# Kernel optimization log

Measured on AMD Instinct MI355X. Metric: run time of the kernel, lower is better.

## Reference

```python
import jax, jax.numpy as jnp
import numpy as np

SR = 16000; NFFT = 1024; HOP = 256; NMELS = 80; GRUH = 256; ZDIM = 16
NBINS = 65; HID = 512; B = 8; TLEN = 160000; PAD = NFFT // 2; IRLEN = 8000

def _consts():
    freqs = np.linspace(0, SR / 2, NFFT // 2 + 1); fsq = freqs ** 2
    aw = (12194.217 ** 2 * fsq ** 2) / ((fsq + 20.6 ** 2) * (fsq + 107.7 ** 2) * (fsq + 737.9 ** 2) * (fsq + 12194.217 ** 2) ** 0.5 + 1e-8)
    h2m = lambda f: 2595.0 * np.log10(1.0 + f / 700.0)
    m2h = lambda m: 700.0 * (10.0 ** (m / 2595.0) - 1.0)
    f_pts = m2h(np.linspace(h2m(0.0), h2m(SR / 2.0), NMELS + 2))
    fd = f_pts[1:] - f_pts[:-1]
    sl = f_pts[None, :] - freqs[:, None]
    fb = np.maximum(0.0, np.minimum(-sl[:, :-2] / fd[:-1], sl[:, 2:] / fd[1:]))
    win = 0.5 - 0.5 * np.cos(2.0 * np.pi * np.arange(NFFT) / NFFT)  # periodic hann
    return jnp.asarray(aw, jnp.float32), jnp.asarray(fb, jnp.float32), jnp.asarray(win, jnp.float32)
AW, MELFB, WIN = _consts()

def _frame(x, size, hop):
    n = (x.shape[-1] - size) // hop + 1
    idx = jnp.arange(n)[:, None] * hop + jnp.arange(size)[None, :]
    return x[:, idx]

def _stft(x):  # [B,T] -> [B, n_frames, 513] complex
    xp = jnp.pad(x, ((0, 0), (PAD, PAD)), mode='reflect')
    return jnp.fft.rfft(_frame(xp, NFFT, HOP) * WIN, axis=-1)

def _istft(spec, length):  # [B, n_frames, 513] -> [B, length]
    fr = jnp.fft.irfft(spec, n=NFFT, axis=-1) * WIN
    n = fr.shape[1]; total = (n - 1) * HOP + NFFT
    idx = (jnp.arange(n)[:, None] * HOP + jnp.arange(NFFT)[None, :]).reshape(-1)
    out = jnp.zeros((fr.shape[0], total), fr.dtype).at[:, idx].add(fr.reshape(fr.shape[0], -1))
    wsq = jnp.zeros((total,), WIN.dtype).at[idx].add(jnp.tile(WIN ** 2, (n,)))
    out = out / jnp.where(wsq > 1e-11, wsq, 1.0)
    return out[:, PAD:PAD + length]

def _lin_interp(x, size):  # torch F.interpolate(mode='linear', align_corners=False) on last axis
    L = x.shape[-1]
    pos = jnp.clip((jnp.arange(size) + 0.5) * (L / size) - 0.5, 0.0, L - 1.0)
    lo = jnp.floor(pos).astype(jnp.int32); hi = jnp.minimum(lo + 1, L - 1); w = pos - lo
    return x[..., lo] * (1.0 - w) + x[..., hi] * w

def _gru(x, wih, whh, bih, bhh):  # torch nn.GRU, batch_first, h0=0
    xp = x @ wih.T + bih
    def step(h, xt):
        gh = h @ whh.T + bhh
        xr, xz, xn = jnp.split(xt, 3, -1); hr, hz, hn = jnp.split(gh, 3, -1)
        r = jax.nn.sigmoid(xr + hr); z = jax.nn.sigmoid(xz + hz)
        nn_ = jnp.tanh(xn + r * hn)
        h = (1.0 - z) * nn_ + z * h
        return h, h
    h0 = jnp.zeros((x.shape[0], whh.shape[1]), x.dtype)
    _, hs = jax.lax.scan(step, h0, jnp.swapaxes(xp, 0, 1))
    return jnp.swapaxes(hs, 0, 1)

def _forward(audio, gender, age, gru_wih, gru_whh, gru_bih, gru_bhh, proj_w, proj_b,
             w0, b0, g0, e0, w1, b1, g1, e1, w2, b2, g2, e2,
             oq_w, oq_b, vt_w, vt_b, nf_w, nf_b, ir):
    # --- pitch via autocorrelation ---
    xp = jnp.pad(audio, ((0, 0), (PAD, PAD)), mode='reflect')
    fr = _frame(xp, NFFT, HOP)
    ps = jnp.abs(jnp.fft.rfft(fr, n=2 * NFFT, axis=-1)) ** 2
    ac = jnp.fft.irfft(ps, n=2 * NFFT, axis=-1)[..., :NFFT]
    ac = ac / (ac[..., :1] + 1e-8)
    min_lag, max_lag = SR // 1000, SR // 50  # 16, 320
    reg = ac[..., min_lag:max_lag]
    mv = jnp.max(reg, -1); mi = jnp.argmax(reg, -1)
    f0 = SR / (mi.astype(jnp.float32) + min_lag + 1e-8)
    f0 = jnp.where(mv < 0.3, 0.0, f0)[..., None]  # [B,F,1]
    # --- loudness + mels ---
    spec = jnp.abs(_stft(audio)) ** 2  # [B,F,513]
    loud = 10.0 * jnp.log10(jnp.mean((spec + 1e-8) * AW, -1, keepdims=True))  # [B,F,1]
    mels = jnp.log(spec @ MELFB + 1e-5)  # [B,F,80]
    mels = (mels - mels.mean(1, keepdims=True)) / jnp.sqrt(mels.var(1, keepdims=True) + 1e-5)
    z = _gru(mels, gru_wih, gru_whh, gru_bih, gru_bhh) @ proj_w.T + proj_b  # [B,F,16]
    Fn = f0.shape[1]
    # --- controller ---
    gb = jnp.broadcast_to(gender[:, None, :], (gender.shape[0], Fn, 2))
    ab = jnp.broadcast_to(age[:, None, :], (age.shape[0], Fn, 1))
    h = jnp.concatenate([z, (jnp.log(f0 + 1e-5) - 4.0) / 4.0, loud / 100.0 + 1.0, gb, ab], -1)
    for W, bb, gm, bt in ((w0, b0, g0, e0), (w1, b1, g1, e1), (w2, b2, g2, e2)):
        h = h @ W.T + bb
        h = (h - h.mean(-1, keepdims=True)) / jnp.sqrt(h.var(-1, keepdims=True) + 1e-5) * gm + bt
        h = jnp.where(h >= 0, h, 0.1 * h)  # LeakyReLU(0.1)
    oq = jax.nn.sigmoid(h @ oq_w.T + oq_b)
    vt = jax.nn.sigmoid(h @ vt_w.T + vt_b)
    nf = jax.nn.sigmoid(h @ nf_w.T + nf_b)
    amp = 10.0 ** (loud / 20.0)
    # --- decoder ---
    L = audio.shape[-1]
    f0u = _lin_interp(f0[..., 0], L); ampu = _lin_interp(amp[..., 0], L); oqu = _lin_interp(oq[..., 0], L)
    phase = jnp.cumsum(f0u / SR, -1); p = phase - jnp.floor(phase)
    oqc = jnp.clip(oqu, 0.1, 0.9)
    pulse = 0.5 * (1.0 - jnp.cos(jnp.pi * p / (oqc + 1e-8)))
    g = pulse * jax.nn.sigmoid((oqc - p) * 100.0)
    glottal = jnp.pad(g[..., 1:] - g[..., :-1], ((0, 0), (1, 0)))
    noise = jax.random.normal(jax.random.key(42), glottal.shape, glottal.dtype)
    def apply_filter(ex, filt):
        es = _stft(ex)  # [B,nf,513]
        ft = _lin_interp(jnp.swapaxes(filt, 1, 2), es.shape[1])  # time interp
        ff = _lin_interp(jnp.swapaxes(ft, 1, 2), es.shape[2])    # bin interp 65->513
        return _istft(es * ff, L)
    dry = (apply_filter(glottal, vt) + apply_filter(noise, nf)) * ampu
    # --- FFT reverb ---
    nconv = int(2 ** int(np.ceil(np.log2(L + IRLEN - 1))))
    wet = jnp.fft.irfft(jnp.fft.rfft(dry, n=nconv) * jnp.fft.rfft(ir, n=nconv), n=nconv)[..., :L]
    return wet, dry

def setup_inputs() -> dict:
    ks = iter(jax.random.split(jax.random.key(0), 48))
    def nrm(shape, s=0.05):
        return jax.random.normal(next(ks), shape, jnp.float32) * s
    inp = {}
    inp['audio'] = jax.random.normal(next(ks), (B, TLEN), jnp.float32)
    inp['gender'] = jax.random.uniform(next(ks), (B, 2), jnp.float32)
    inp['age'] = jax.random.uniform(next(ks), (B, 1), jnp.float32)
    inp['gru_wih'] = nrm((3 * GRUH, NMELS)); inp['gru_whh'] = nrm((3 * GRUH, GRUH))
    inp['gru_bih'] = jnp.zeros((3 * GRUH,), jnp.float32); inp['gru_bhh'] = jnp.zeros((3 * GRUH,), jnp.float32)
    inp['proj_w'] = nrm((ZDIM, GRUH)); inp['proj_b'] = jnp.zeros((ZDIM,), jnp.float32)
    din = ZDIM + 5
    inp['w0'] = nrm((HID, din)); inp['b0'] = jnp.zeros((HID,), jnp.float32)
    inp['g0'] = jnp.ones((HID,), jnp.float32); inp['e0'] = jnp.zeros((HID,), jnp.float32)
    inp['w1'] = nrm((HID, HID)); inp['b1'] = jnp.zeros((HID,), jnp.float32)
    inp['g1'] = jnp.ones((HID,), jnp.float32); inp['e1'] = jnp.zeros((HID,), jnp.float32)
    inp['w2'] = nrm((HID, HID)); inp['b2'] = jnp.zeros((HID,), jnp.float32)
    inp['g2'] = jnp.ones((HID,), jnp.float32); inp['e2'] = jnp.zeros((HID,), jnp.float32)
    inp['oq_w'] = nrm((1, HID)); inp['oq_b'] = jnp.zeros((1,), jnp.float32)
    inp['vt_w'] = nrm((NBINS, HID)); inp['vt_b'] = jnp.zeros((NBINS,), jnp.float32)
    inp['nf_w'] = nrm((NBINS, HID)); inp['nf_b'] = jnp.zeros((NBINS,), jnp.float32)
    decay = jnp.exp(-jnp.linspace(0.0, 5.0, IRLEN))
    inp['ir'] = jax.random.normal(next(ks), (IRLEN,), jnp.float32) * 0.1 * decay
    return inp

def reference(audio, gender, age, gru_wih, gru_whh, gru_bih, gru_bhh, proj_w, proj_b,
              w0, b0, g0, e0, w1, b1, g1, e1, w2, b2, g2, e2,
              oq_w, oq_b, vt_w, vt_b, nf_w, nf_b, ir):
    return _forward(audio, gender, age, gru_wih, gru_whh, gru_bih, gru_bhh, proj_w, proj_b,
                    w0, b0, g0, e0, w1, b1, g1, e1, w2, b2, g2, e2,
                    oq_w, oq_b, vt_w, vt_b, nf_w, nf_b, ir)
```

## Files before the change

kernel.cpp:

```cpp
#include <hip/hip_runtime.h>
#include <math.h>

#define SRF 16000.0f
#define HOP 256
#define FRM 626
#define BB 8
#define TLEN 160000
#define NFRM (BB*FRM)
#define NCONV 262144
#define ACCLEN 161024
#define GCH 40

constexpr size_t oWIN   = 0;
constexpr size_t oTW    = oWIN + 1024;
constexpr size_t oDIAG  = oTW + 1024;
constexpr size_t oTWF   = oDIAG + 16;
constexpr size_t oTWC   = oTWF + 1024;
constexpr size_t oAW    = oTWC + 1024;
constexpr size_t oMELFB = oAW + 513;
constexpr size_t oWSQI  = oMELFB + 513*80;
constexpr size_t oWIHT  = oWSQI + ACCLEN;
constexpr size_t oW0T   = oWIHT + 80*768;
constexpr size_t oW1T   = oW0T + 21*512;
constexpr size_t oW2T   = oW1T + 512*512;
constexpr size_t oVTT   = oW2T + 512*512;
constexpr size_t oNFT   = oVTT + 512*65;
constexpr size_t oF0    = oNFT + 512*65;
constexpr size_t oLOUD  = oF0 + NFRM;
constexpr size_t oOQ    = oLOUD + NFRM;
constexpr size_t oVT    = oOQ + NFRM;
constexpr size_t oNF    = oVT + (size_t)NFRM*65;
constexpr size_t oGLOT  = oNF + (size_t)NFRM*65;
constexpr size_t oNOISE = oGLOT + (size_t)BB*TLEN;
constexpr size_t oACC   = oNOISE + (size_t)BB*TLEN;
constexpr size_t oCONVA = oACC + (size_t)BB*ACCLEN;
constexpr size_t oEND   = oCONVA + (size_t)5*NCONV*2;
constexpr size_t oXP    = oEND;
constexpr size_t oGSUM  = oXP + (size_t)NFRM*768;
constexpr size_t oGPRE  = oGSUM + 320;
constexpr size_t oEND2  = oGPRE + 640;
constexpr size_t oCONVB = oWSQI;
constexpr size_t oMEL = oCONVA;
constexpr size_t oHS  = oMEL + (size_t)NFRM*80;

constexpr long R_WIN=1024, R_TW=512, R_TWF=512, R_TWC=512, R_AW=513, R_MELFB=41040,
  R_WSQI=161024, R_WIHT=61440, R_W0T=10752, R_W1T=262144, R_W2T=262144,
  R_VTT=33280, R_NFT=33280, R_IR=NCONV;
constexpr long INIT_TOTAL = R_WIN+R_TW+R_TWF+R_TWC+R_AW+R_MELFB+R_WSQI+R_WIHT+R_W0T+
  R_W1T+R_W2T+R_VTT+R_NFT+R_IR;

constexpr int NOISEB = 313;
constexpr int ZACCB  = 315;
constexpr int MEGA_BLOCKS = 1 + NFRM + NOISEB + ZACCB;

typedef float f32x4 __attribute__((ext_vector_type(4)));
typedef __bf16 bf16x8 __attribute__((ext_vector_type(8)));
typedef short short8 __attribute__((ext_vector_type(8)));
#define MFMA_BF16 __builtin_amdgcn_mfma_f32_16x16x32_bf16

__device__ inline int mirror_idx(int j) {
  if (j < 0) j = -j;
  if (j >= TLEN) j = 2*TLEN - 2 - j;
  return j;
}
__device__ inline float sigm(float x) { return 1.0f/(1.0f + expf(-x)); }
__device__ inline unsigned short f2bf(float x) {
  unsigned u = __float_as_uint(x);
  return (unsigned short)((u + 0x7FFFu + ((u >> 16) & 1u)) >> 16);
}
__device__ inline float tanh_fast(float x) {
  return 1.0f - 2.0f/(__expf(2.0f*x) + 1.0f);
}

__device__ inline float interpF(const float* v, int i) {
  float pos = ((float)i + 0.5f) * (626.0f/160000.0f) - 0.5f;
  pos = fminf(fmaxf(pos, 0.0f), 625.0f);
  int lo = (int)floorf(pos);
  int hi = min(lo + 1, 625);
  float w = pos - (float)lo;
  return v[lo]*(1.0f - w) + v[hi]*w;
}
__device__ inline float interp65(const float* v, int k) {
  float pos = ((float)k + 0.5f) * (65.0f/513.0f) - 0.5f;
  pos = fminf(fmaxf(pos, 0.0f), 64.0f);
  int lo = (int)floorf(pos);
  int hi = min(lo + 1, 64);
  float w = pos - (float)lo;
  return v[lo]*(1.0f - w) + v[hi]*w;
}
__device__ inline float gwave(float ph, float oqu) {
  float p = ph - floorf(ph);
  float oqc = fminf(fmaxf(oqu, 0.1f), 0.9f);
  float pulse = 0.5f*(1.0f - cosf(3.14159265358979f * p / (oqc + 1e-8f)));
  float gs = 1.0f/(1.0f + __expf(-(oqc - p)*100.0f));
  return pulse*gs;
}

template<int LOGN, int TS>
__device__ inline void fft2(float2* c, const float2* tw, int tid, int nthr, bool inv) {
  constexpr int N = 1 << LOGN;
  for (int s = 1; s <= LOGN; ++s) {
    const int half = 1 << (s-1);
    const int tstep = (N >> s) * TS;
    for (int bf = tid; bf < (N>>1); bf += nthr) {
      int jj = bf & (half-1);
      int i0 = ((bf >> (s-1)) << s) + jj;
      int i1 = i0 + half;
      float2 wv = tw[jj*tstep];
      float wi = inv ? -wv.y : wv.y;
      float2 u = c[i0], v = c[i1];
      float tr  = v.x*wv.x - v.y*wi;
      float tci = v.x*wi  + v.y*wv.x;
      c[i0] = make_float2(u.x + tr, u.y + tci);
      c[i1] = make_float2(u.x - tr, u.y - tci);
    }
    __syncthreads();
  }
}

__device__ inline void threefry2x32(unsigned k0, unsigned k1, unsigned x0, unsigned x1,
                                    unsigned& o0, unsigned& o1) {
  unsigned ks2 = k0 ^ k1 ^ 0x1BD11BDAu;
  x0 += k0; x1 += k1;
#define TF_R(r) { x0 += x1; x1 = (x1<<(r)) | (x1>>(32-(r))); x1 ^= x0; }
  TF_R(13) TF_R(15) TF_R(26) TF_R(6)
  x0 += k1; x1 += ks2 + 1u;
  TF_R(17) TF_R(29) TF_R(16) TF_R(24)
  x0 += ks2; x1 += k0 + 2u;
  TF_R(13) TF_R(15) TF_R(26) TF_R(6)
  x0 += k0; x1 += k1 + 3u;
  TF_R(17) TF_R(29) TF_R(16) TF_R(24)
  x0 += k1; x1 += ks2 + 4u;
  TF_R(13) TF_R(15) TF_R(26) TF_R(6)
  x0 += ks2; x1 += k0 + 5u;
#undef TF_R
  o0 = x0; o1 = x1;
}

__device__ inline float erfinv_f(float x) {
  float w = -log1pf(-x*x);
  float p;
  if (w < 5.0f) {
    w = w - 2.5f;
    p = 2.81022636e-08f;
    p = fmaf(p, w, 3.43273939e-07f);
    p = fmaf(p, w, -3.5233877e-06f);
    p = fmaf(p, w, -4.39150654e-06f);
    p = fmaf(p, w, 0.00021858087f);
    p = fmaf(p, w, -0.00125372503f);
    p = fmaf(p, w, -0.00417768164f);
    p = fmaf(p, w, 0.246640727f);
    p = fmaf(p, w, 1.50140941f);
  } else {
    w = sqrtf(w) - 3.0f;
    p = -0.000200214257f;
    p = fmaf(p, w, 0.000100950558f);
    p = fmaf(p, w, 0.00134934322f);
    p = fmaf(p, w, -0.00367342844f);
    p = fmaf(p, w, 0.00573950773f);
    p = fmaf(p, w, -0.0076224613f);
    p = fmaf(p, w, 0.00943887047f);
    p = fmaf(p, w, 1.00167406f);
    p = fmaf(p, w, 2.83297682f);
  }
  return p*x;
}
__device__ inline float normal_from_bits(unsigned bits) {
  float f = __uint_as_float((bits >> 9) | 0x3F800000u) - 1.0f;
  float x = fmaxf(-0.99999994f, fmaf(f, 1.99999994f, -0.99999994f));
  return 1.41421356237f * erfinv_f(x);
}

__device__ inline double mel_fpt(int j) {
  double mmax = 2595.0 * log10(1.0 + 8000.0/700.0);
  return 700.0 * (pow(10.0, (mmax * (double)j / 81.0) / 2595.0) - 1.0);
}

__global__ void k_init(float* W, const float* wih, const float* w0,
                       const float* w1, const float* w2, const float* vtw, const float* nfw,
                       const float* ir) {
  long id = (long)blockIdx.x*256 + threadIdx.x;
  if (id < R_WIN) {
    double w = 0.5 - 0.5*cos(2.0*M_PI*(double)id/1024.0);
    W[oWIN+id] = (float)w; return;
  } id -= R_WIN;
  if (id < R_TW) {
    double a = -2.0*M_PI*(double)id/1024.0;
    W[oTW+2*id] = (float)cos(a); W[oTW+2*id+1] = (float)sin(a); return;
  } id -= R_TW;
  if (id < R_TWF) {
    double a = -2.0*M_PI*(double)id/262144.0;
    W[oTWF+2*id] = (float)cos(a); W[oTWF+2*id+1] = (float)sin(a); return;
  } id -= R_TWF;
  if (id < R_TWC) {
    double a = -2.0*M_PI*(double)id/512.0;
    W[oTWC+2*id] = (float)cos(a); W[oTWC+2*id+1] = (float)sin(a); return;
  } id -= R_TWC;
  if (id < R_AW) {
    double fr = (double)id*(8000.0/512.0); double fsq = fr*fr;
    double num = 12194.217*12194.217*fsq*fsq;
    double den = (fsq+20.6*20.6)*(fsq+107.7*107.7)*(fsq+737.9*737.9)*sqrt(fsq+12194.217*12194.217) + 1e-8;
    W[oAW+id] = (float)(num/den); return;
  } id -= R_AW;
  if (id < R_MELFB) {
    int k = (int)(id/80), m = (int)(id%80);
    double fk = (double)k*(8000.0/512.0);
    double f0p = mel_fpt(m), f1p = mel_fpt(m+1), f2p = mel_fpt(m+2);
    double lower = (fk - f0p)/(f1p - f0p);
    double upper = (f2p - fk)/(f2p - f1p);
    double v = fmax(0.0, fmin(lower, upper));
    W[oMELFB+id] = (float)v; return;
  } id -= R_MELFB;
  if (id < R_WSQI) {
    int t = (int)id;
    int n1 = t/256; if (n1 > 625) n1 = 625;
    int n0t = t - 1023 + 255; int n0 = (n0t > 0) ? n0t/256 : 0;
    double s = 0.0;
    for (int n = n0; n <= n1; ++n) {
      int o = t - n*256;
      double wv = 0.5 - 0.5*cos(2.0*M_PI*(double)o/1024.0);
      s += wv*wv;
    }
    float sf = (float)s;
    W[oWSQI+t] = (sf > 1e-11f) ? (1.0f/sf) : 1.0f; return;
  } id -= R_WSQI;
  if (id < R_WIHT) { long k = id/768, g = id%768; W[oWIHT+id] = wih[g*80+k];  return; } id -= R_WIHT;
  if (id < R_W0T)  { long d = id/512, j = id%512; W[oW0T+id] = w0[j*21+d];   return; } id -= R_W0T;
  if (id < R_W1T)  { long k = id/512, j = id%512; W[oW1T+id] = w1[j*512+k];  return; } id -= R_W1T;
  if (id < R_W2T)  { long k = id/512, j = id%512; W[oW2T+id] = w2[j*512+k];  return; } id -= R_W2T;
  if (id < R_VTT)  { long k = id/65,  m = id%65;  W[oVTT+id] = vtw[m*512+k]; return; } id -= R_VTT;
  if (id < R_NFT)  { long k = id/65,  m = id%65;  W[oNFT+id] = nfw[m*512+k]; return; } id -= R_NFT;
  if (id < R_IR) {
    size_t base = oCONVA + 2*((size_t)4*NCONV + id);
    W[base] = (id < 8000) ? ir[id] : 0.0f; W[base+1] = 0.0f; return;
  }
}

__global__ __launch_bounds__(256) void k_stft_mel(const float* audio, float* W) {
  int blk = blockIdx.x; int b = blk/FRM, f = blk%FRM; int tid = threadIdx.x;
  __shared__ float2 cb[1024];
  __shared__ float spec[513];
  __shared__ float redbuf[4];
  const float* arow = audio + (size_t)b*TLEN;
  const float2* tw = (const float2*)(W + oTW);
  for (int i = tid; i < 1024; i += 256) {
    float v = arow[mirror_idx(f*256 + i - 512)] * W[oWIN + i];
    int pos = __brev((unsigned)i) >> 22;
    cb[pos] = make_float2(v, 0.f);
  }
  __syncthreads();
  fft2<10,1>(cb, tw, tid, 256, false);
  for (int k = tid; k < 513; k += 256) { float2 z = cb[k]; spec[k] = z.x*z.x + z.y*z.y; }
  __syncthreads();
  float part = 0.f;
  for (int k = tid; k < 513; k += 256) part += (spec[k] + 1e-8f) * W[oAW + k];
  for (int off = 32; off; off >>= 1) part += __shfl_down(part, off, 64);
  if ((tid & 63) == 0) redbuf[tid >> 6] = part;
  __syncthreads();
  if (tid == 0) {
    float s = redbuf[0]+redbuf[1]+redbuf[2]+redbuf[3];
    W[oLOUD + blk] = 10.0f * log10f(s / 513.0f);
  }
  for (int m = tid; m < 80; m += 256) {
    double f0p = mel_fpt(m), f2p = mel_fpt(m + 2);
    int klo = (int)(f0p * (512.0/8000.0)); if (klo < 0) klo = 0;
    int khi = (int)(f2p * (512.0/8000.0)) + 1; if (khi > 512) khi = 512;
    float s = 0.f;
    for (int k = klo; k <= khi; ++k) s += spec[k]*W[oMELFB + (size_t)k*80 + m];
    W[oMEL + (size_t)blk*80 + m] = logf(s + 1e-5f);
  }
}

__global__ void k_melnorm(float* W) {
  int id = blockIdx.x*256 + threadIdx.x;
  if (id >= BB*80) return;
  int b = id/80, m = id%80;
  double s = 0.0, ss = 0.0;
  for (int f = 0; f < FRM; ++f) {
    double v = W[oMEL + ((size_t)b*FRM + f)*80 + m];
    s += v; ss += v*v;
  }
  double mean = s/FRM;
  double var = ss/FRM - mean*mean;
  float mu = (float)mean;
  float rstd = (float)(1.0/sqrt(var + 1e-5));
  for (int f = 0; f < FRM; ++f) {
    size_t idx = oMEL + ((size_t)b*FRM + f)*80 + m;
    W[idx] = (W[idx] - mu)*rstd;
  }
}

__global__ void k_xp(float* W, const float* bih) {
  size_t id = (size_t)blockIdx.x*256 + threadIdx.x;
  if (id >= (size_t)NFRM*768) return;
  int g = (int)(id % 768);
  size_t q = id / 768;
  const float* mrow = W + oMEL + q*80;
  float acc = bih[g];
  for (int k = 0; k < 80; ++k) acc = fmaf(mrow[k], W[oWIHT + (size_t)k*768 + g], acc);
  W[oXP + q*768 + g] = acc;
}

__global__ __launch_bounds__(512, 2) void k_mega(float* W, const float* audio,
                                                 const float* whh, const float* bhh) {
  __shared__ unsigned short sB[32768];
  __shared__ unsigned short sA[4096];
  __shared__ float sGT[9216];
  __shared__ float fr4[4][1032];
  __shared__ float wpow[8];
  __shared__ float wmax[8];
  __shared__ int   wmaxi[8];
  int tid = threadIdx.x;
  int blk = blockIdx.x;

  if (blk == 0) {
    int w = tid >> 6, l = tid & 63;
    const float* XP = W + oXP;
    float* HS = W + oHS;

    for (int idx = tid; idx < 32768; idx += 512) {
      int lcol = idx >> 8, k = idx & 255;
      int gcol = 96*(lcol >> 4) + 80 + (lcol & 15);
      sB[lcol*256 + (k ^ ((lcol & 7) << 3))] = f2bf(whh[(size_t)gcol*256 + k]);
    }
    for (int idx = tid; idx < 4096; idx += 512) sA[idx] = 0;

    int cl = l & 15, khalf = (l >> 4) * 8;
    bf16x8 bw[40];
    #pragma unroll
    for (int t2 = 0; t2 < 5; ++t2) {
      int col = 96*w + 16*t2 + cl;
      #pragma unroll
      for (int kk = 0; kk < 8; ++kk) {
        const float* src = whh + (size_t)col*256 + kk*32 + khalf;
        short8 tmp;
        #pragma unroll
        for (int j = 0; j < 8; ++j) tmp[j] = (short)f2bf(src[j]);
        bw[t2*8 + kk] = __builtin_bit_cast(bf16x8, tmp);
      }
    }

    int g = tid & 255, bbase = tid >> 8;
    float bh_r = bhh[g], bh_z = bhh[256 + g], bh_n = bhh[512 + g];
    float hprev[4] = {0.f, 0.f, 0.f, 0.f};
    int aXor = (cl & 7) << 3;
    int lcol5 = w*16 + cl;
    int rowg = l >> 4;
    int colb = 96*w + cl;
    int gtw = colb*12 + rowg*4;
    int gtr0 = g*12 + 4*bbase;
    int gtr1 = (256 + g)*12 + 4*bbase;
    int gtr2 = (512 + g)*12 + 4*bbase;

    __syncthreads();

#define LDA(kk) (*(const bf16x8*)&sA[(cl)*256 + (((kk)*32 + khalf) ^ aXor)])
#define LDB(kk) (*(const bf16x8*)&sB[(lcol5)*256 + (((kk)*32 + khalf) ^ aXor)])
#define STEPK(A_, kk) \
      c0 = MFMA_BF16(A_, bw[0*8+(kk)], c0, 0, 0, 0); \
      c1 = MFMA_BF16(A_, bw[1*8+(kk)], c1, 0, 0, 0); \
      c2 = MFMA_BF16(A_, bw[2*8+(kk)], c2, 0, 0, 0); \
      c3 = MFMA_BF16(A_, bw[3*8+(kk)], c3, 0, 0, 0); \
      c4 = MFMA_BF16(A_, bw[4*8+(kk)], c4, 0, 0, 0); \
      c5 = MFMA_BF16(A_, LDB(kk), c5, 0, 0, 0);

    for (int t = 0; t < FRM; ++t) {
      float xr[4], xz[4], xn[4];
      #pragma unroll
      for (int j = 0; j < 4; ++j) {
        const float* xpp = XP + ((size_t)(4*bbase + j)*FRM + t)*768 + g;
        xr[j] = xpp[0]; xz[j] = xpp[256]; xn[j] = xpp[512];
      }
      f32x4 c0 = {0,0,0,0}, c1 = {0,0,0,0}, c2 = {0,0,0,0};
      f32x4 c3 = {0,0,0,0}, c4 = {0,0,0,0}, c5 = {0,0,0,0};
      bf16x8 a0 = LDA(0), a1 = LDA(1), a2 = LDA(2), a3 = LDA(3);
      STEPK(a0, 0) STEPK(a1, 1) STEPK(a2, 2) STEPK(a3, 3)
      a0 = LDA(4); a1 = LDA(5); a2 = LDA(6); a3 = LDA(7);
      STEPK(a0, 4) STEPK(a1, 5) STEPK(a2, 6) STEPK(a3, 7)
      if (rowg < 3) {
        *(f32x4*)&sGT[gtw + 0*192]  = c0;
        *(f32x4*)&sGT[gtw + 1*192]  = c1;
        *(f32x4*)&sGT[gtw + 2*192]  = c2;
        *(f32x4*)&sGT[gtw + 3*192]  = c3;
        *(f32x4*)&sGT[gtw + 4*192]  = c4;
        *(f32x4*)&sGT[gtw + 5*192]  = c5;
      }
      __syncthreads();
      f32x4 rv = *(const f32x4*)&sGT[gtr0];
      f32x4 zv = *(const f32x4*)&sGT[gtr1];
      f32x4 nv = *(const f32x4*)&sGT[gtr2];
      #pragma unroll
      for (int j = 0; j < 4; ++j) {
        int bb = 4*bbase + j;
        float r = 1.0f/(1.0f + __expf(-(xr[j] + rv[j] + bh_r)));
        float z = 1.0f/(1.0f + __expf(-(xz[j] + zv[j] + bh_z)));
        float nn = tanh_fast(xn[j] + r*(nv[j] + bh_n));
        float h = (1.0f - z)*nn + z*hprev[j];
        hprev[j] = h;
        HS[((size_t)bb*FRM + t)*256 + g] = h;
        sA[bb*256 + (g ^ ((bb & 7) << 3))] = f2bf(h);
      }
      __syncthreads();
    }
#undef LDA
#undef LDB
#undef STEPK
    return;
  }
  blk -= 1;

  if (blk < NFRM) {
    int b = blk/FRM, f = blk%FRM;
    const float* arow = audio + (size_t)b*TLEN;
    for (int idx = tid; idx < 4*1032; idx += 512) {
      int s = idx/1032, i = idx - s*1032;
      int j = i + s;
      fr4[s][i] = (j < 1024) ? arow[mirror_idx(f*256 + j - 512)] : 0.f;
    }
    __syncthreads();
    int lane = tid & 63, wv = tid >> 6;
    float p = 0.f;
    for (int i = tid; i < 1024; i += 512) { float x = fr4[0][i]; p += x*x; }
    for (int off = 32; off; off >>= 1) p += __shfl_down(p, off, 64);
    if (lane == 0) wpow[wv] = p;
    float vbest = -1e30f; int ibest = tid;
    if (tid < 304) {
      int lag = 16 + tid;
      int s = lag & 3, base = lag - s;
      int qmax = (1023 - lag) >> 2;
      float acc = 0.f;
      for (int q = 0; q <= qmax; ++q) {
        float4 u = *(const float4*)&fr4[0][4*q];
        float4 v = *(const float4*)&fr4[s][base + 4*q];
        acc += u.x*v.x + u.y*v.y + u.z*v.z + u.w*v.w;
      }
      vbest = acc;
    }
    for (int off = 32; off; off >>= 1) {
      float v2 = __shfl_down(vbest, off, 64);
      int i2 = __shfl_down(ibest, off, 64);
      if (v2 > vbest || (v2 == vbest && i2 < ibest)) { vbest = v2; ibest = i2; }
    }
    if (lane == 0) { wmax[wv] = vbest; wmaxi[wv] = ibest; }
    __syncthreads();
    if (tid == 0) {
      float ac0 = 0.f;
      #pragma unroll
      for (int q = 0; q < 8; ++q) ac0 += wpow[q];
      float bv = wmax[0]; int bi = wmaxi[0];
      #pragma unroll
      for (int q = 1; q < 8; ++q) {
        if (wmax[q] > bv || (wmax[q] == bv && wmaxi[q] < bi)) { bv = wmax[q]; bi = wmaxi[q]; }
      }
      float inv = 1.0f/(ac0 + 1e-8f);
      float best = bv*inv;
      W[oF0 + (size_t)blk] = (best < 0.3f) ? 0.0f : (SRF/(float)(bi + 16));
    }
    return;
  }
  blk -= NFRM;

  if (blk < NOISEB) {
    size_t base = (size_t)blk*4096;
    #pragma unroll
    for (int j = 0; j < 8; ++j) {
      size_t p = base + (size_t)j*512 + tid;
      if (p < (size_t)BB*TLEN) {
        unsigned o0, o1;
        threefry2x32(0u, 42u, 0u, (unsigned)p, o0, o1);
        W[oNOISE + p] = normal_from_bits(o0 ^ o1);
      }
    }
    return;
  }
  blk -= NOISEB;

  {
    size_t base = (size_t)blk*4096;
    #pragma unroll
    for (int j = 0; j < 8; ++j) {
      size_t p = base + (size_t)j*512 + tid;
      if (p < (size_t)BB*ACCLEN) W[oACC + p] = 0.0f;
    }
  }
}

__device__ inline void ln_lrelu(float acc[8], float gj, float ej, float out[8][512],
                                float wred[8][8][2], float stat[8][2],
                                int tid, int lane, int wv, int j) {
  #pragma unroll
  for (int i = 0; i < 8; ++i) {
    float s = acc[i], ss = acc[i]*acc[i];
    for (int off = 32; off; off >>= 1) { s += __shfl_down(s, off, 64); ss += __shfl_down(ss, off, 64); }
    if (lane == 0) { wred[i][wv][0] = s; wred[i][wv][1] = ss; }
  }
  __syncthreads();
  if (tid < 8) {
    float s = 0.f, ss = 0.f;
    #pragma unroll
    for (int w = 0; w < 8; ++w) { s += wred[tid][w][0]; ss += wred[tid][w][1]; }
    float mean = s/512.0f;
    float var = ss/512.0f - mean*mean;
    stat[tid][0] = mean;
    stat[tid][1] = 1.0f/sqrtf(var + 1e-5f);
  }
  __syncthreads();
  #pragma unroll
  for (int i = 0; i < 8; ++i) {
    float v = (acc[i] - stat[i][0])*stat[i][1]*gj + ej;
    out[i][j] = (v >= 0.f) ? v : 0.1f*v;
  }
}

__global__ __launch_bounds__(512) void k_mlp(float* W, const float* gender, const float* age,
    const float* projw, const float* projb,
    const float* b0, const float* g0, const float* e0,
    const float* b1, const float* g1, const float* e1,
    const float* b2, const float* g2, const float* e2,
    const float* oqw, const float* oqb, const float* vtb, const float* nfb) {
  __shared__ float hbuf[8][256];
  __shared__ float in0[8][21];
  __shared__ float actA[8][512];
  __shared__ float actB[8][512];
  __shared__ float wred[8][8][2];
  __shared__ float stat[8][2];
  int tid = threadIdx.x; int q0 = blockIdx.x*8;
  for (int x = tid; x < 2048; x += 512) {
    int i = x >> 8, k = x & 255;
    hbuf[i][k] = W[oHS + ((size_t)(q0 + i))*256 + k];
  }
  __syncthreads();
  if (tid < 128) {
    int i = tid >> 4, zi = tid & 15;
    float a = projb[zi];
    for (int k = 0; k < 256; ++k) a = fmaf(hbuf[i][k], projw[zi*256 + k], a);
    in0[i][zi] = a;
  } else if (tid < 168) {
    int x = tid - 128; int i = x/5, d = 16 + x%5;
    int q = q0 + i; int b = q/FRM;
    float v;
    if (d == 16) v = (logf(W[oF0 + q] + 1e-5f) - 4.0f)*0.25f;
    else if (d == 17) v = W[oLOUD + q]/100.0f + 1.0f;
    else if (d == 18) v = gender[b*2];
    else if (d == 19) v = gender[b*2 + 1];
    else v = age[b];
    in0[i][d] = v;
  }
  __syncthreads();
  int j = tid, lane = tid & 63, wv = tid >> 6;
  float acc[8];
  #pragma unroll
  for (int i = 0; i < 8; ++i) acc[i] = b0[j];
  for (int d = 0; d < 21; ++d) {
    float w = W[oW0T + (size_t)d*512 + j];
    #pragma unroll
    for (int i = 0; i < 8; ++i) acc[i] = fmaf(in0[i][d], w, acc[i]);
  }
  ln_lrelu(acc, g0[j], e0[j], actA, wred, stat, tid, lane, wv, j);
  __syncthreads();
  #pragma unroll
  for (int i = 0; i < 8; ++i) acc[i] = b1[j];
  for (int k = 0; k < 512; ++k) {
    float w = W[oW1T + (size_t)k*512 + j];
    #pragma unroll
    for (int i = 0; i < 8; ++i) acc[i] = fmaf(actA[i][k], w, acc[i]);
  }
  ln_lrelu(acc, g1[j], e1[j], actB, wred, stat, tid, lane, wv, j);
  __syncthreads();
  #pragma unroll
  for (int i = 0; i < 8; ++i) acc[i] = b2[j];
  for (int k = 0; k < 512; ++k) {
    float w = W[oW2T + (size_t)k*512 + j];
    #pragma unroll
    for (int i = 0; i < 8; ++i) acc[i] = fmaf(actB[i][k], w, acc[i]);
  }
  ln_lrelu(acc, g2[j], e2[j], actA, wred, stat, tid, lane, wv, j);
  __syncthreads();
  for (int x = tid; x < 520; x += 512) {
    int i = x/65, m = x%65;
    float a = vtb[m], a2 = nfb[m];
    for (int k = 0; k < 512; ++k) {
      float h = actA[i][k];
      a  = fmaf(h, W[oVTT + (size_t)k*65 + m], a);
      a2 = fmaf(h, W[oNFT + (size_t)k*65 + m], a2);
    }
    W[oVT + (size_t)(q0+i)*65 + m] = sigm(a);
    W[oNF + (size_t)(q0+i)*65 + m] = sigm(a2);
  }
  if (tid < 8) {
    float a = oqb[0];
    for (int k = 0; k < 512; ++k) a = fmaf(actA[tid][k], oqw[k], a);
    W[oOQ + q0 + tid] = sigm(a);
  }
}

__global__ __launch_bounds__(256) void k_gsum(float* W) {
  int blk = blockIdx.x; int b = blk/GCH, c = blk%GCH; int tid = threadIdx.x;
  __shared__ float ws[4];
  const float* f0r = W + oF0 + (size_t)b*FRM;
  int i0 = c*4096 + tid*16;
  float s = 0.f;
  #pragma unroll
  for (int j = 0; j < 16; ++j) {
    int i = i0 + j;
    if (i < TLEN) s += interpF(f0r, i)*(1.0f/SRF);
  }
  for (int off = 32; off; off >>= 1) s += __shfl_down(s, off, 64);
  if ((tid & 63) == 0) ws[tid >> 6] = s;
  __syncthreads();
  if (tid == 0) W[oGSUM + (size_t)b*GCH + c] = ws[0]+ws[1]+ws[2]+ws[3];
}

__global__ void k_gscan(float* W) {
  if (blockIdx.x == 0 && threadIdx.x == 0) {
    double* P = (double*)(W + oGPRE);
    for (int b = 0; b < BB; ++b) {
      double a = 0.0;
      for (int c = 0; c < GCH; ++c) {
        P[b*GCH + c] = a;
        a += (double)W[oGSUM + (size_t)b*GCH + c];
      }
    }
  }
}

__global__ __launch_bounds__(256) void k_gapply(float* W) {
  int blk = blockIdx.x; int b = blk/GCH, c = blk%GCH; int tid = threadIdx.x;
  __shared__ float wss[4];
  __shared__ float lastw[4];
  const float* f0r = W + oF0 + (size_t)b*FRM;
  const float* oqr = W + oOQ + (size_t)b*FRM;
  float* grow = W + oGLOT + (size_t)b*TLEN;
  double P = ((const double*)(W + oGPRE))[b*GCH + c];
  int i0 = c*4096 + tid*16;
  int lane = tid & 63, wv = tid >> 6;
  float v[16]; float ts = 0.f;
  #pragma unroll
  for (int j = 0; j < 16; ++j) {
    int i = i0 + j;
    float x = (i < TLEN) ? interpF(f0r, i)*(1.0f/SRF) : 0.f;
    v[j] = x; ts += x;
  }
  float sc = ts;
  #pragma unroll
  for (int off = 1; off < 64; off <<= 1) {
    float o = __shfl_up(sc, off, 64);
    if (lane >= off) sc += o;
  }
  if (lane == 63) wss[wv] = sc;
  __syncthreads();
  float wpre = 0.f;
  for (int q = 0; q < wv; ++q) wpre += wss[q];
  double ph0 = P + (double)(wpre + sc - ts);
  float run = 0.f; float gq[16];
  #pragma unroll
  for (int j = 0; j < 16; ++j) {
    int i = i0 + j;
    run += v[j];
    float ph = (float)(ph0 + (double)run);
    gq[j] = gwave(ph, interpF(oqr, min(i, TLEN-1)));
  }
  float prev = __shfl_up(gq[15], 1, 64);
  if (lane == 63) lastw[wv] = gq[15];
  __syncthreads();
  if (lane == 0) {
    if (wv > 0) prev = lastw[wv - 1];
    else if (i0 > 0) prev = gwave((float)P, interpF(oqr, i0 - 1));
    else prev = 0.f;
  }
  #pragma unroll
  for (int j = 0; j < 16; ++j) {
    int i = i0 + j;
    if (i < TLEN) {
      float gl = (j == 0) ? prev : gq[j-1];
      grow[i] = (i == 0) ? 0.f : (gq[j] - gl);
    }
  }
}

__global__ __launch_bounds__(256) void k_filtsynth(float* W) {
  int blk = blockIdx.x; int b = blk/FRM, f = blk%FRM; int tid = threadIdx.x;
  __shared__ float2 cZ[1024], cS[1024];
  __shared__ float fvt[65], fnf[65];
  const float* grow = W + oGLOT + (size_t)b*TLEN;
  const float* nrow = W + oNOISE + (size_t)b*TLEN;
  const float2* tw = (const float2*)(W + oTW);
  for (int i = tid; i < 1024; i += 256) {
    int si = mirror_idx(f*256 + i - 512);
    float wv = W[oWIN + i];
    int pos = __brev((unsigned)i) >> 22;
    cZ[pos] = make_float2(grow[si]*wv, nrow[si]*wv);
  }
  if (tid < 65) {
    fvt[tid] = W[oVT + ((size_t)b*FRM + f)*65 + tid];
    fnf[tid] = W[oNF + ((size_t)b*FRM + f)*65 + tid];
  }
  __syncthreads();
  fft2<10,1>(cZ, tw, tid, 256, false);
  for (int k = tid; k <= 512; k += 256) {
    int km = (1024 - k) & 1023;
    float2 z1 = cZ[k], z2 = cZ[km];
    float Gr = 0.5f*(z1.x + z2.x), Gi = 0.5f*(z1.y - z2.y);
    float Nr = 0.5f*(z1.y + z2.y), Ni = 0.5f*(z2.x - z1.x);
    float fv = interp65(fvt, k), fn = interp65(fnf, k);
    float Sr = Gr*fv + Nr*fn, Si = Gi*fv + Ni*fn;
    cS[__brev((unsigned)k) >> 22] = make_float2(Sr, Si);
    if (km != k) cS[__brev((unsigned)km) >> 22] = make_float2(Sr, -Si);
  }
  __syncthreads();
  fft2<10,1>(cS, tw, tid, 256, true);
  float* arow = W + oACC + (size_t)b*ACCLEN + (size_t)f*256;
  for (int i = tid; i < 1024; i += 256) {
    float xv = cS[i].x*(1.0f/1024.0f)*W[oWIN + i];
    atomicAdd(arow + i, xv);
  }
}

__global__ void k_dry(float* W, float* dout) {
  size_t id = (size_t)blockIdx.x*256 + threadIdx.x;
  if (id >= (size_t)4*NCONV) return;
  int t = (int)(id / NCONV);
  int n = (int)(id % NCONV);
  float dv0 = 0.f, dv1 = 0.f;
  if (n < TLEN) {
    float pos = ((float)n + 0.5f) * (626.0f/160000.0f) - 0.5f;
    pos = fminf(fmaxf(pos, 0.0f), 625.0f);
    int lo = (int)floorf(pos);
    int hi = min(lo + 1, 625);
    float wgt = pos - (float)lo;
    float wsq = W[oWSQI + 512 + n];
    #pragma unroll
    for (int q = 0; q < 2; ++q) {
      int b = 2*t + q;
      float val = W[oACC + (size_t)b*ACCLEN + 512 + n] * wsq;
      const float* lrow = W + oLOUD + (size_t)b*FRM;
      float a0 = exp10f(lrow[lo]*0.05f);
      float a1 = exp10f(lrow[hi]*0.05f);
      float dv = val*(a0*(1.0f - wgt) + a1*wgt);
      if (q == 0) dv0 = dv; else dv1 = dv;
      dout[(size_t)BB*TLEN + (size_t)b*TLEN + n] = dv;
    }
  }
  ((float2*)(W + oCONVA))[id] = make_float2(dv0, dv1);
}

__global__ __launch_bounds__(256) void k_conv_f1(const float* in, float* out,
                                                 const float* tw, const float* twf,
                                                 const float* twc) {
  int blk = blockIdx.x; int t = blk >> 9; int bcol = blk & 511; int tid = threadIdx.x;
  __shared__ float2 cb[512];
  const float2* src = (const float2*)in + (size_t)t*NCONV;
  for (int a = tid; a < 512; a += 256) {
    int pos = __brev((unsigned)a) >> 23;
    cb[pos] = src[(size_t)a*512 + bcol];
  }
  __syncthreads();
  fft2<9,2>(cb, (const float2*)tw, tid, 256, false);
  float2* dst = (float2*)out + (size_t)t*NCONV + (size_t)bcol*512;
  for (int k1 = tid; k1 < 512; k1 += 256) {
    unsigned m = (unsigned)bcol * (unsigned)k1;
    float2 tc = ((const float2*)twc)[m >> 9];
    float2 tf = ((const float2*)twf)[m & 511];
    float wr = tc.x*tf.x - tc.y*tf.y;
    float wi = tc.x*tf.y + tc.y*tf.x;
    float2 v = cb[k1];
    dst[k1] = make_float2(v.x*wr - v.y*wi, v.x*wi + v.y*wr);
  }
}

__global__ __launch_bounds__(256) void k_conv_f2(const float* in, float* out, const float* tw) {
  int blk = blockIdx.x; int t = blk >> 9; int k1 = blk & 511; int tid = threadIdx.x;
  __shared__ float2 cb[512];
  const float2* src = (const float2*)in + (size_t)t*NCONV;
  for (int bb2 = tid; bb2 < 512; bb2 += 256) {
    int pos = __brev((unsigned)bb2) >> 23;
    cb[pos] = src[(size_t)bb2*512 + k1];
  }
  __syncthreads();
  fft2<9,2>(cb, (const float2*)tw, tid, 256, false);
  float2* dst = (float2*)out + (size_t)t*NCONV;
  for (int k2 = tid; k2 < 512; k2 += 256) {
    dst[(size_t)k1 + 512*(size_t)k2] = cb[k2];
  }
}

__global__ __launch_bounds__(256) void k_conv_f2w(const float* in, float* dout, const float* tw) {
  int blk = blockIdx.x; int t = blk >> 9; int k1 = blk & 511; int tid = threadIdx.x;
  __shared__ float2 cb[512];
  const float2* src = (const float2*)in + (size_t)t*NCONV;
  for (int bb2 = tid; bb2 < 512; bb2 += 256) {
    int pos = __brev((unsigned)bb2) >> 23;
    cb[pos] = src[(size_t)bb2*512 + k1];
  }
  __syncthreads();
  fft2<9,2>(cb, (const float2*)tw, tid, 256, false);
  float* d0 = dout + (size_t)(2*t)*TLEN;
  float* d1 = dout + (size_t)(2*t + 1)*TLEN;
  for (int k2 = tid; k2 < 512; k2 += 256) {
    int n = k1 + 512*k2;
    if (n < TLEN) {
      float2 V = cb[k2];
      d0[n] = V.x * (1.0f/262144.0f);
      d1[n] = -V.y * (1.0f/262144.0f);
    }
  }
}

__global__ void k_mul(float* W) {
  constexpr size_t HALF = NCONV/2;
  size_t id = (size_t)blockIdx.x*256 + threadIdx.x;
  if (id >= (size_t)4*(HALF + 1)) return;
  int t = (int)(id / (HALF + 1));
  size_t k = id % (HALF + 1);
  size_t km = (NCONV - k) & (NCONV - 1);
  float2* A = (float2*)(W + oCONVA);
  float2 z1 = A[(size_t)t*NCONV + k];
  float2 z2 = A[(size_t)t*NCONV + km];
  float2 c  = A[(size_t)4*NCONV + k];
  float X0r = 0.5f*(z1.x + z2.x), X0i = 0.5f*(z1.y - z2.y);
  float X1r = 0.5f*(z1.y + z2.y), X1i = 0.5f*(z2.x - z1.x);
  float P0r = X0r*c.x - X0i*c.y, P0i = X0r*c.y + X0i*c.x;
  float P1r = X1r*c.x - X1i*c.y, P1i = X1r*c.y + X1i*c.x;
  A[(size_t)t*NCONV + k] = make_float2(P0r - P1i, -(P0i + P1r));
  if (km != k) {
    A[(size_t)t*NCONV + km] = make_float2(P0r + P1i, P0i - P1r);
  }
}

extern "C" void kernel_launch(void* const* d_in, const int* in_sizes, int n_in,
                              void* d_out, int out_size, void* d_ws, size_t ws_size,
                              hipStream_t stream) {
  (void)in_sizes; (void)n_in; (void)out_size; (void)ws_size;
  const float* audio  = (const float*)d_in[0];
  const float* gender = (const float*)d_in[1];
  const float* age    = (const float*)d_in[2];
  const float* wih    = (const float*)d_in[3];
  const float* whh    = (const float*)d_in[4];
  const float* bih    = (const float*)d_in[5];
  const float* bhh    = (const float*)d_in[6];
  const float* projw  = (const float*)d_in[7];
  const float* projb  = (const float*)d_in[8];
  const float* w0     = (const float*)d_in[9];
  const float* b0     = (const float*)d_in[10];
  const float* g0     = (const float*)d_in[11];
  const float* e0     = (const float*)d_in[12];
  const float* w1     = (const float*)d_in[13];
  const float* b1     = (const float*)d_in[14];
  const float* g1     = (const float*)d_in[15];
  const float* e1     = (const float*)d_in[16];
  const float* w2     = (const float*)d_in[17];
  const float* b2     = (const float*)d_in[18];
  const float* g2     = (const float*)d_in[19];
  const float* e2     = (const float*)d_in[20];
  const float* oqw    = (const float*)d_in[21];
  const float* oqb    = (const float*)d_in[22];
  const float* vtw    = (const float*)d_in[23];
  const float* vtb    = (const float*)d_in[24];
  const float* nfw    = (const float*)d_in[25];
  const float* nfb    = (const float*)d_in[26];
  const float* ir     = (const float*)d_in[27];
  float* W = (float*)d_ws;
  float* dout = (float*)d_out;

  k_init<<<(int)((INIT_TOTAL + 255)/256), 256, 0, stream>>>(W, wih, w0, w1, w2, vtw, nfw, ir);
  k_stft_mel<<<NFRM, 256, 0, stream>>>(audio, W);
  k_melnorm<<<3, 256, 0, stream>>>(W);
  k_xp<<<(int)(((size_t)NFRM*768 + 255)/256), 256, 0, stream>>>(W, bih);
  k_mega<<<MEGA_BLOCKS, 512, 0, stream>>>(W, audio, whh, bhh);
  k_mlp<<<NFRM/8, 512, 0, stream>>>(W, gender, age, projw, projb,
                                    b0, g0, e0, b1, g1, e1, b2, g2, e2, oqw, oqb, vtb, nfb);
  k_gsum<<<BB*GCH, 256, 0, stream>>>(W);
  k_gscan<<<1, 64, 0, stream>>>(W);
  k_gapply<<<BB*GCH, 256, 0, stream>>>(W);
  k_filtsynth<<<NFRM, 256, 0, stream>>>(W);
  k_dry<<<(int)(((size_t)4*NCONV + 255)/256), 256, 0, stream>>>(W, dout);
  k_conv_f1<<<5*512, 256, 0, stream>>>(W + oCONVA, W + oCONVB, W + oTW, W + oTWF, W + oTWC);
  k_conv_f2<<<5*512, 256, 0, stream>>>(W + oCONVB, W + oCONVA, W + oTW);
  k_mul<<<(int)(((size_t)4*(NCONV/2 + 1) + 255)/256), 256, 0, stream>>>(W);
  k_conv_f1<<<4*512, 256, 0, stream>>>(W + oCONVA, W + oCONVB, W + oTW, W + oTWF, W + oTWC);
  k_conv_f2w<<<4*512, 256, 0, stream>>>(W + oCONVB, dout, W + oTW);
}
```

Baseline: 2.098 ms.

## Keep all GRU recurrent weights in registers and interleave XP by batch

The sixth recurrent weight tile moves from a shared-memory bf16 copy into registers, which removes the sB staging buffer and its per-step LDS loads on the serial GRU critical path. The input-projection buffer XP is re-laid out as [t][gate][batch], so each thread fetches its four batch values per gate with one float4 load instead of twelve strided scalar loads. Together these cut per-step latency in the sequential recurrence. The cost is higher register pressure (48 bf16x8 vectors), which could spill under the 512-thread, two-blocks-per-SM launch bound. k_xp now writes in the interleaved order, which gives it a different and less coalesced access pattern on its reads.

```diff
diff --git a/kernel.cpp b/kernel.cpp
--- a/kernel.cpp
+++ b/kernel.cpp
@@ -36,7 +36,7 @@
 constexpr size_t oCONVA = oACC + (size_t)BB*ACCLEN;
 constexpr size_t oEND   = oCONVA + (size_t)5*NCONV*2;
 constexpr size_t oXP    = oEND;
-constexpr size_t oGSUM  = oXP + (size_t)NFRM*768;
+constexpr size_t oGSUM  = oXP + (size_t)FRM*768*8;
 constexpr size_t oGPRE  = oGSUM + 320;
 constexpr size_t oEND2  = oGPRE + 640;
 constexpr size_t oCONVB = oWSQI;
@@ -292,18 +292,18 @@
 
 __global__ void k_xp(float* W, const float* bih) {
   size_t id = (size_t)blockIdx.x*256 + threadIdx.x;
-  if (id >= (size_t)NFRM*768) return;
-  int g = (int)(id % 768);
-  size_t q = id / 768;
-  const float* mrow = W + oMEL + q*80;
+  if (id >= (size_t)FRM*768*8) return;
+  int b = (int)(id & 7);
+  int g = (int)((id >> 3) % 768);
+  int t = (int)(id / (768*8));
+  const float* mrow = W + oMEL + ((size_t)b*FRM + t)*80;
   float acc = bih[g];
   for (int k = 0; k < 80; ++k) acc = fmaf(mrow[k], W[oWIHT + (size_t)k*768 + g], acc);
-  W[oXP + q*768 + g] = acc;
+  W[oXP + id] = acc;
 }
 
 __global__ __launch_bounds__(512, 2) void k_mega(float* W, const float* audio,
                                                  const float* whh, const float* bhh) {
-  __shared__ unsigned short sB[32768];
   __shared__ unsigned short sA[4096];
   __shared__ float sGT[9216];
   __shared__ float fr4[4][1032];
@@ -318,17 +318,12 @@
     const float* XP = W + oXP;
     float* HS = W + oHS;
 
-    for (int idx = tid; idx < 32768; idx += 512) {
-      int lcol = idx >> 8, k = idx & 255;
-      int gcol = 96*(lcol >> 4) + 80 + (lcol & 15);
-      sB[lcol*256 + (k ^ ((lcol & 7) << 3))] = f2bf(whh[(size_t)gcol*256 + k]);
-    }
     for (int idx = tid; idx < 4096; idx += 512) sA[idx] = 0;
 
     int cl = l & 15, khalf = (l >> 4) * 8;
-    bf16x8 bw[40];
+    bf16x8 bw[48];
     #pragma unroll
-    for (int t2 = 0; t2 < 5; ++t2) {
+    for (int t2 = 0; t2 < 6; ++t2) {
       int col = 96*w + 16*t2 + cl;
       #pragma unroll
       for (int kk = 0; kk < 8; ++kk) {
@@ -344,10 +339,12 @@
     float bh_r = bhh[g], bh_z = bhh[256 + g], bh_n = bhh[512 + g];
     float hprev[4] = {0.f, 0.f, 0.f, 0.f};
     int aXor = (cl & 7) << 3;
-    int lcol5 = w*16 + cl;
     int rowg = l >> 4;
     int colb = 96*w + cl;
     int gtw = colb*12 + rowg*4;
+    size_t xpr = (size_t)g*8 + 4*bbase;
+    size_t xpz = (size_t)(256 + g)*8 + 4*bbase;
+    size_t xpn = (size_t)(512 + g)*8 + 4*bbase;
     int gtr0 = g*12 + 4*bbase;
     int gtr1 = (256 + g)*12 + 4*bbase;
     int gtr2 = (512 + g)*12 + 4*bbase;
@@ -355,22 +352,19 @@
     __syncthreads();
 
 #define LDA(kk) (*(const bf16x8*)&sA[(cl)*256 + (((kk)*32 + khalf) ^ aXor)])
-#define LDB(kk) (*(const bf16x8*)&sB[(lcol5)*256 + (((kk)*32 + khalf) ^ aXor)])
 #define STEPK(A_, kk) \
       c0 = MFMA_BF16(A_, bw[0*8+(kk)], c0, 0, 0, 0); \
       c1 = MFMA_BF16(A_, bw[1*8+(kk)], c1, 0, 0, 0); \
       c2 = MFMA_BF16(A_, bw[2*8+(kk)], c2, 0, 0, 0); \
       c3 = MFMA_BF16(A_, bw[3*8+(kk)], c3, 0, 0, 0); \
       c4 = MFMA_BF16(A_, bw[4*8+(kk)], c4, 0, 0, 0); \
-      c5 = MFMA_BF16(A_, LDB(kk), c5, 0, 0, 0);
+      c5 = MFMA_BF16(A_, bw[5*8+(kk)], c5, 0, 0, 0);
 
     for (int t = 0; t < FRM; ++t) {
-      float xr[4], xz[4], xn[4];
-      #pragma unroll
-      for (int j = 0; j < 4; ++j) {
-        const float* xpp = XP + ((size_t)(4*bbase + j)*FRM + t)*768 + g;
-        xr[j] = xpp[0]; xz[j] = xpp[256]; xn[j] = xpp[512];
-      }
+      size_t xbase = (size_t)t*6144;
+      float4 xr4 = *(const float4*)&XP[xbase + xpr];
+      float4 xz4 = *(const float4*)&XP[xbase + xpz];
+      float4 xn4 = *(const float4*)&XP[xbase + xpn];
       f32x4 c0 = {0,0,0,0}, c1 = {0,0,0,0}, c2 = {0,0,0,0};
       f32x4 c3 = {0,0,0,0}, c4 = {0,0,0,0}, c5 = {0,0,0,0};
       bf16x8 a0 = LDA(0), a1 = LDA(1), a2 = LDA(2), a3 = LDA(3);
@@ -392,9 +386,9 @@
       #pragma unroll
       for (int j = 0; j < 4; ++j) {
         int bb = 4*bbase + j;
-        float r = 1.0f/(1.0f + __expf(-(xr[j] + rv[j] + bh_r)));
-        float z = 1.0f/(1.0f + __expf(-(xz[j] + zv[j] + bh_z)));
-        float nn = tanh_fast(xn[j] + r*(nv[j] + bh_n));
+        float r = 1.0f/(1.0f + __expf(-(xr4[j] + rv[j] + bh_r)));
+        float z = 1.0f/(1.0f + __expf(-(xz4[j] + zv[j] + bh_z)));
+        float nn = tanh_fast(xn4[j] + r*(nv[j] + bh_n));
         float h = (1.0f - z)*nn + z*hprev[j];
         hprev[j] = h;
         HS[((size_t)bb*FRM + t)*256 + g] = h;
@@ -403,7 +397,6 @@
       __syncthreads();
     }
 #undef LDA
-#undef LDB
 #undef STEPK
     return;
   }
@@ -865,7 +858,7 @@
   k_init<<<(int)((INIT_TOTAL + 255)/256), 256, 0, stream>>>(W, wih, w0, w1, w2, vtw, nfw, ir);
   k_stft_mel<<<NFRM, 256, 0, stream>>>(audio, W);
   k_melnorm<<<3, 256, 0, stream>>>(W);
-  k_xp<<<(int)(((size_t)NFRM*768 + 255)/256), 256, 0, stream>>>(W, bih);
+  k_xp<<<(int)(((size_t)FRM*768*8 + 255)/256), 256, 0, stream>>>(W, bih);
   k_mega<<<MEGA_BLOCKS, 512, 0, stream>>>(W, audio, whh, bhh);
   k_mlp<<<NFRM/8, 512, 0, stream>>>(W, gender, age, projw, projb,
                                     b0, g0, e0, b1, g1, e1, b2, g2, e2, oqw, oqb, vtb, nfb);
```

New measurement: 2.482 ms. 18.3% more time.
